# Kernel tuning notes

Measured on AMD Instinct MI355X. Metric: run time of the kernel, lower is better.

The kernel has to match this reference:

```python
import jax, jax.numpy as jnp
import numpy as np

TAU = 1.0
EPS = 1e-5


def _gcn_sparse(x, src, dst, ew, W, b, n):
    # PyG GCNConv: add self-loops (weight 1), sym-normalize, aggregate src->dst
    deg = jax.ops.segment_sum(ew, dst, num_segments=n) + 1.0
    dinv = jnp.where(deg > 0, jax.lax.rsqrt(deg), 0.0)
    h = x @ W
    coef = dinv[src] * ew * dinv[dst]              # [E]
    out = jax.ops.segment_sum(h[src] * coef[:, None], dst, num_segments=n)
    out = out + h * (dinv * dinv)[:, None]         # self-loop term
    return out + b


def _gcn_dense(x, A, W, b):
    # x: [B,N,d], A: [B,N,N] with A[b,i,j] = weight of edge j->i
    n = A.shape[-1]
    Ah = A + jnp.eye(n, dtype=A.dtype)
    deg = Ah.sum(-1)
    dinv = jnp.where(deg > 0, jax.lax.rsqrt(deg), 0.0)
    An = dinv[:, :, None] * Ah * dinv[:, None, :]
    return jnp.einsum('bij,bjd->bid', An, x @ W) + b


def _bn_silu(x, g, be, axes):
    # BatchNorm over node axis (training-mode batch stats, biased var) + SiLU
    m = x.mean(axes, keepdims=True)
    v = x.var(axes, keepdims=True)
    return jax.nn.silu(g * (x - m) * jax.lax.rsqrt(v + EPS) + be)


def setup_inputs() -> dict:
    key = jax.random.key(0)
    ks = jax.random.split(key, 12)
    B, NPG, EPER = 32, 1024, 16384
    CIN, C, K1, K2, OUT = 64, 128, 128, 32, 10
    N, E = B * NPG, B * EPER
    ei = jax.random.randint(ks[0], (2, E), 0, NPG, dtype=jnp.int32)
    off = jnp.repeat(jnp.arange(B, dtype=jnp.int32) * NPG, EPER)
    edge_index = ei + off[None, :]
    x = jax.random.normal(ks[1], (N, CIN), jnp.float32)
    batch = jnp.repeat(jnp.arange(B, dtype=jnp.int32), NPG)
    batch_ptr = jnp.arange(B + 1, dtype=jnp.int32) * NPG
    p = lambda k, s: jax.random.normal(k, s, jnp.float32) * 0.05
    return dict(
        x=x, edge_index=edge_index, batch=batch, batch_ptr=batch_ptr,
        w1a=p(ks[2], (CIN, C)), b1a=jnp.zeros((C,)), g1a=jnp.ones((C,)), be1a=jnp.zeros((C,)),
        w1b=p(ks[3], (C, C)), b1b=jnp.zeros((C,)), g1b=jnp.ones((C,)), be1b=jnp.zeros((C,)),
        wp1=p(ks[4], (C, K1)), bp1=jnp.zeros((K1,)),
        w2a=p(ks[5], (C, C)), b2a=jnp.zeros((C,)), g2a=jnp.ones((C,)), be2a=jnp.zeros((C,)),
        w2b=p(ks[6], (C, C)), b2b=jnp.zeros((C,)), g2b=jnp.ones((C,)), be2b=jnp.zeros((C,)),
        wp2=p(ks[7], (C, K2)), bp2=jnp.zeros((K2,)),
        wl=p(ks[8], (C, OUT)), bl=jnp.zeros((OUT,)))


def reference(x, edge_index, batch, batch_ptr,
              w1a, b1a, g1a, be1a, w1b, b1b, g1b, be1b, wp1, bp1,
              w2a, b2a, g2a, be2a, w2b, b2b, g2b, be2b, wp2, bp2,
              wl, bl):
    n = x.shape[0]
    B = batch_ptr.shape[0] - 1
    npg = n // B                                    # uniform nodes per graph
    src, dst = edge_index[0], edge_index[1]
    ew = jnp.ones((edge_index.shape[1],), x.dtype)  # edge_weight=None -> ones

    # ---- stack 1: sparse GCN residual blocks + stochastic pool ----
    h = _bn_silu(_gcn_sparse(x, src, dst, ew, w1a, b1a, n), g1a, be1a, 0)
    h = h + _bn_silu(_gcn_sparse(h, src, dst, ew, w1b, b1b, n), g1b, be1b, 0)
    s = jax.nn.softmax(_gcn_sparse(h, src, dst, ew, wp1, bp1, n) / TAU, -1)  # [n,K1]
    s3 = s.reshape(B, npg, -1)
    x2 = jnp.einsum('bnc,bnd->bcd', s3, h.reshape(B, npg, -1))   # s^T x  [B,K1,C]
    t = jax.ops.segment_sum(s[src] * ew[:, None], dst, num_segments=n)  # A s
    A2 = jnp.einsum('bnc,bnk->bck', s3, t.reshape(B, npg, -1))   # s^T A s [B,K1,K1]

    # ---- stack 2: dense GCN on pooled graph + stochastic pool ----
    h2 = _bn_silu(_gcn_dense(x2, A2, w2a, b2a), g2a, be2a, (0, 1))
    h2 = h2 + _bn_silu(_gcn_dense(h2, A2, w2b, b2b), g2b, be2b, (0, 1))
    s2 = jax.nn.softmax(_gcn_dense(h2, A2, wp2, bp2) / TAU, -1)  # [B,K1,K2]
    x3 = jnp.einsum('bnc,bnd->bcd', s2, h2)                      # [B,K2,C]

    # global mean pool over nodes per graph, linear, log_softmax
    g = x3.mean(axis=1)
    out = jax.nn.log_softmax(g @ wl + bl, axis=1)
    # aux losses are multiplied by 0 in the original forward -> exact zero
    return (out, jnp.zeros((), x.dtype))
```

## Files before the change

### kernel.cpp

```cpp
#include <hip/hip_runtime.h>
#include <cmath>

#define KSPLIT 8
#define ELL_ST 80

typedef __attribute__((ext_vector_type(8))) short short8;
typedef __attribute__((ext_vector_type(4))) float float4v;

static __device__ __forceinline__ unsigned short f2bf(float f){
  union { float f; unsigned u; } c; c.f = f;
  unsigned r = c.u + 0x7fff + ((c.u >> 16) & 1);
  return (unsigned short)(r >> 16);
}
static __device__ __forceinline__ float u2f(unsigned u){
  union { unsigned u; float f; } c; c.u = u; return c.f;
}
static __device__ __forceinline__ float silu(float y){ return y/(1.f+__expf(-y)); }

static __device__ __forceinline__ void coef_prologue(const float* __restrict__ stats,
                                                     const float* __restrict__ gamma,
                                                     const float* __restrict__ beta,
                                                     float invM, float* lds, int tbase){
  int t = threadIdx.x - tbase;
  if(t >= 0 && t < 128){
    float s = 0.f, q = 0.f;
    #pragma unroll
    for(int k=0;k<8;k++){ s += stats[k*128+t]; q += stats[1024 + k*128+t]; }
    float m = s*invM;
    float v = q*invM - m*m;
    float sc = gamma[t]*rsqrtf(v + 1e-5f);
    lds[t] = sc;
    lds[128+t] = beta[t] - m*sc;
  }
}

__global__ void k_fill_wt(const int* __restrict__ src, const int* __restrict__ dst,
                          int* __restrict__ cursor, int* __restrict__ esrc, int E,
                          const float* __restrict__ w1a, const float* __restrict__ w1b,
                          const float* __restrict__ wp1, const float* __restrict__ w2a,
                          const float* __restrict__ w2b,
                          unsigned short* __restrict__ t1a, unsigned short* __restrict__ t1b,
                          unsigned short* __restrict__ tp1, unsigned short* __restrict__ t2a,
                          unsigned short* __restrict__ t2b,
                          const float* __restrict__ xin, unsigned short* __restrict__ xb,
                          int NX, int CIN){
  int i = blockIdx.x*256 + threadIdx.x;
  if(i < E){
    int d = dst[i];
    int p = atomicAdd(&cursor[d], 1);
    if(p < ELL_ST) esrc[(size_t)d*ELL_ST + p] = src[i];
  } else {
    int j = i - E;
    int n1 = CIN*128, n2 = 128*128;
    if(j >= 0 && j < n1){
      int k = j >> 7, c = j & 127;
      t1a[(size_t)c*CIN + k] = f2bf(w1a[j]);
    } else if(j >= n1 && j < n1+n2){
      int jj = j - n1; int k = jj >> 7, c = jj & 127;
      t1b[(size_t)c*128 + k] = f2bf(w1b[jj]);
    } else if(j >= n1+n2 && j < n1+2*n2){
      int jj = j - n1 - n2; int k = jj >> 7, c = jj & 127;
      tp1[(size_t)c*128 + k] = f2bf(wp1[jj]);
    } else if(j >= n1+2*n2 && j < n1+3*n2){
      int jj = j - n1 - 2*n2; int k = jj >> 7, c = jj & 127;
      t2a[(size_t)c*128 + k] = f2bf(w2a[jj]);
    } else if(j >= n1+3*n2 && j < n1+4*n2){
      int jj = j - n1 - 3*n2; int k = jj >> 7, c = jj & 127;
      t2b[(size_t)c*128 + k] = f2bf(w2b[jj]);
    } else if(j >= n1+4*n2 && j < n1+4*n2+NX){
      int jj = j - n1 - 4*n2;
      xb[jj] = f2bf(xin[jj]);
    }
  }
}

template<bool ABF16>
__global__ void k_gemm_mfma(const void* __restrict__ A, const void* __restrict__ A2,
                            const unsigned short* __restrict__ Bt,
                            unsigned short* __restrict__ Cb,
                            unsigned short* __restrict__ Hout, int M, int K,
                            const int* __restrict__ rowdeg,
                            const float* __restrict__ rowscale,
                            const float* __restrict__ stA, const float* __restrict__ gA,
                            const float* __restrict__ beA,
                            const float* __restrict__ stB, const float* __restrict__ gB,
                            const float* __restrict__ beB, float invM){
  __shared__ unsigned short Abf[64][40];
  __shared__ unsigned short Bbf[128][40];
  __shared__ float lcA[256], lcB[256];
  int tid = threadIdx.x;
  if(stA) coef_prologue(stA, gA, beA, invM, lcA, 0);
  if(stB) coef_prologue(stB, gB, beB, invM, lcB, 128);
  if(stA || stB) __syncthreads();
  int wv = tid >> 6, lane = tid & 63;
  int quad = lane >> 4, l16 = lane & 15;
  int row0 = blockIdx.x*64;
  int sr = tid >> 2, sk = (tid & 3)*8;
  int srb = tid >> 1, skb = (tid & 1)*16;
  float4v acc[8] = {};
  for(int kt=0; kt<K; kt+=32){
    uint4 pk;
    if(ABF16){
      const unsigned short* ap = (const unsigned short*)A + (size_t)(row0+sr)*K + kt + sk;
      uint4 u = *(const uint4*)ap;
      if(stA){
        float va[8];
        va[0]=u2f(u.x<<16); va[1]=u2f(u.x&0xffff0000u);
        va[2]=u2f(u.y<<16); va[3]=u2f(u.y&0xffff0000u);
        va[4]=u2f(u.z<<16); va[5]=u2f(u.z&0xffff0000u);
        va[6]=u2f(u.w<<16); va[7]=u2f(u.w&0xffff0000u);
        if(stB){
          const unsigned short* bp = (const unsigned short*)A2 + (size_t)(row0+sr)*K + kt + sk;
          uint4 v = *(const uint4*)bp;
          float vb[8];
          vb[0]=u2f(v.x<<16); vb[1]=u2f(v.x&0xffff0000u);
          vb[2]=u2f(v.y<<16); vb[3]=u2f(v.y&0xffff0000u);
          vb[4]=u2f(v.z<<16); vb[5]=u2f(v.z&0xffff0000u);
          vb[6]=u2f(v.w<<16); vb[7]=u2f(v.w&0xffff0000u);
          #pragma unroll
          for(int i=0;i<8;i++){
            int c = kt+sk+i;
            va[i] = silu(lcA[c]*va[i] + lcA[128+c]) + silu(lcB[c]*vb[i] + lcB[128+c]);
          }
        } else {
          #pragma unroll
          for(int i=0;i<8;i++){
            int c = kt+sk+i;
            va[i] = silu(lcA[c]*va[i] + lcA[128+c]);
          }
        }
        pk.x = (unsigned)f2bf(va[0]) | ((unsigned)f2bf(va[1])<<16);
        pk.y = (unsigned)f2bf(va[2]) | ((unsigned)f2bf(va[3])<<16);
        pk.z = (unsigned)f2bf(va[4]) | ((unsigned)f2bf(va[5])<<16);
        pk.w = (unsigned)f2bf(va[6]) | ((unsigned)f2bf(va[7])<<16);
      } else {
        pk = u;
      }
    } else {
      const float* ap = (const float*)A + (size_t)(row0+sr)*K + kt + sk;
      float va[8];
      *(float4*)&va[0] = *(const float4*)ap;
      *(float4*)&va[4] = *(const float4*)(ap+4);
      if(stA){
        #pragma unroll
        for(int i=0;i<8;i++){
          int c = kt+sk+i;
          va[i] = silu(lcA[c]*va[i] + lcA[128+c]);
        }
      }
      pk.x = (unsigned)f2bf(va[0]) | ((unsigned)f2bf(va[1])<<16);
      pk.y = (unsigned)f2bf(va[2]) | ((unsigned)f2bf(va[3])<<16);
      pk.z = (unsigned)f2bf(va[4]) | ((unsigned)f2bf(va[5])<<16);
      pk.w = (unsigned)f2bf(va[6]) | ((unsigned)f2bf(va[7])<<16);
    }
    *(uint4*)&Abf[sr][sk] = pk;
    if(Hout)
      *(uint4*)&Hout[(size_t)(row0+sr)*128 + kt + sk] = pk;
    *(uint4*)&Bbf[srb][skb]   = *(const uint4*)&Bt[(size_t)srb*K + kt + skb];
    *(uint4*)&Bbf[srb][skb+8] = *(const uint4*)&Bt[(size_t)srb*K + kt + skb + 8];
    __syncthreads();
    short8 af = *(const short8*)&Abf[wv*16 + l16][quad*8];
    #pragma unroll
    for(int t=0;t<8;t++){
      short8 bf = *(const short8*)&Bbf[t*16 + l16][quad*8];
      acc[t] = __builtin_amdgcn_mfma_f32_16x16x32_bf16(af, bf, acc[t], 0, 0, 0);
    }
    __syncthreads();
  }
  float scr[4];
  #pragma unroll
  for(int r=0;r<4;r++){
    int grow = row0 + wv*16 + quad*4 + r;
    scr[r] = rowdeg ? rsqrtf((float)rowdeg[grow] + 1.0f) : (rowscale ? rowscale[grow] : 1.f);
  }
  #pragma unroll
  for(int t=0;t<8;t++){
    #pragma unroll
    for(int r=0;r<4;r++){
      int grow = row0 + wv*16 + quad*4 + r;
      Cb[(size_t)grow*128 + t*16 + l16] = f2bf(acc[t][r]*scr[r]);
    }
  }
}

template<bool DO_SOFTMAX, bool GCN, bool STATS, bool BF16IN, bool BF16OUT>
__global__ void k_gather(const int* __restrict__ degc, const int* __restrict__ esrc,
                         const void* __restrict__ hWs,
                         const float* __restrict__ bias, float* __restrict__ out,
                         float* __restrict__ stats){
  __shared__ float lsum[4][128];
  __shared__ float lsq[4][128];
  const unsigned short* h16 = (const unsigned short*)hWs;
  const float* h32 = (const float*)hWs;
  int wave = threadIdx.x >> 6;
  int lane = threadIdx.x & 63;
  int bid = blockIdx.x;
  int d = ((bid & 7) << 12) | ((bid >> 3) << 2) | wave;
  int grp = lane >> 5;
  int c4 = (lane & 31)*4;
  int dgr = degc[d];
  int cnt = dgr > ELL_ST ? ELL_ST : dgr;
  cnt = __builtin_amdgcn_readfirstlane(cnt);
  const int* row = esrc + (size_t)d*ELL_ST;

  auto loadrow = [&](int s)->float4{
    if(BF16IN){
      uint2 u = *(const uint2*)&h16[(size_t)s*128 + c4];
      float4 v;
      v.x = u2f(u.x << 16); v.y = u2f(u.x & 0xffff0000u);
      v.z = u2f(u.y << 16); v.w = u2f(u.y & 0xffff0000u);
      return v;
    } else {
      return *(const float4*)&h32[(size_t)s*128 + c4];
    }
  };

  float4 a0 = {0.f,0.f,0.f,0.f}, a1 = {0.f,0.f,0.f,0.f};
  float4 a2 = {0.f,0.f,0.f,0.f}, a3 = {0.f,0.f,0.f,0.f};
  if(GCN && grp == 0)
    a0 = loadrow(d);
  for(int base=0; base<cnt; base+=32){
    int m = cnt - base; if(m > 32) m = 32;
    int idx = (lane < m) ? row[base + lane] : 0;
    int full = m & ~7;
    int j0 = 0;
    for(; j0 < full; j0 += 8){
      int s0 = __shfl(idx, j0+grp);
      int s1 = __shfl(idx, j0+grp+2);
      int s2 = __shfl(idx, j0+grp+4);
      int s3 = __shfl(idx, j0+grp+6);
      float4 v0 = loadrow(s0);
      float4 v1 = loadrow(s1);
      float4 v2 = loadrow(s2);
      float4 v3 = loadrow(s3);
      a0.x+=v0.x; a0.y+=v0.y; a0.z+=v0.z; a0.w+=v0.w;
      a1.x+=v1.x; a1.y+=v1.y; a1.z+=v1.z; a1.w+=v1.w;
      a2.x+=v2.x; a2.y+=v2.y; a2.z+=v2.z; a2.w+=v2.w;
      a3.x+=v3.x; a3.y+=v3.y; a3.z+=v3.z; a3.w+=v3.w;
    }
    if(j0 < m){
      int jj0 = j0+grp, jj1 = j0+grp+2, jj2 = j0+grp+4, jj3 = j0+grp+6;
      int s0 = __shfl(idx, jj0 < m ? jj0 : 0);
      int s1 = __shfl(idx, jj1 < m ? jj1 : 0);
      int s2 = __shfl(idx, jj2 < m ? jj2 : 0);
      int s3 = __shfl(idx, jj3 < m ? jj3 : 0);
      if(jj0 < m){ float4 v = loadrow(s0);
        a0.x+=v.x; a0.y+=v.y; a0.z+=v.z; a0.w+=v.w; }
      if(jj1 < m){ float4 v = loadrow(s1);
        a1.x+=v.x; a1.y+=v.y; a1.z+=v.z; a1.w+=v.w; }
      if(jj2 < m){ float4 v = loadrow(s2);
        a2.x+=v.x; a2.y+=v.y; a2.z+=v.z; a2.w+=v.w; }
      if(jj3 < m){ float4 v = loadrow(s3);
        a3.x+=v.x; a3.y+=v.y; a3.z+=v.z; a3.w+=v.w; }
    }
  }
  float4 acc;
  acc.x = (a0.x+a1.x)+(a2.x+a3.x);
  acc.y = (a0.y+a1.y)+(a2.y+a3.y);
  acc.z = (a0.z+a1.z)+(a2.z+a3.z);
  acc.w = (a0.w+a1.w)+(a2.w+a3.w);
  acc.x += __shfl_xor(acc.x, 32);
  acc.y += __shfl_xor(acc.y, 32);
  acc.z += __shfl_xor(acc.z, 32);
  acc.w += __shfl_xor(acc.w, 32);
  float4 val = acc;
  if(GCN){
    float dv = rsqrtf((float)dgr + 1.0f);
    float4 bi = *(const float4*)&bias[c4];
    val.x = dv*acc.x + bi.x; val.y = dv*acc.y + bi.y;
    val.z = dv*acc.z + bi.z; val.w = dv*acc.w + bi.w;
  }
  if(DO_SOFTMAX){
    float mx = fmaxf(fmaxf(val.x,val.y), fmaxf(val.z,val.w));
    #pragma unroll
    for(int o=1;o<32;o<<=1) mx = fmaxf(mx, __shfl_xor(mx,o));
    float4 e; e.x=__expf(val.x-mx); e.y=__expf(val.y-mx);
    e.z=__expf(val.z-mx); e.w=__expf(val.w-mx);
    float s = e.x+e.y+e.z+e.w;
    #pragma unroll
    for(int o=1;o<32;o<<=1) s += __shfl_xor(s,o);
    float inv = 1.f/s;
    val.x=e.x*inv; val.y=e.y*inv; val.z=e.z*inv; val.w=e.w*inv;
  }
  if(grp == 0){
    if(BF16OUT){
      unsigned short* o16 = (unsigned short*)out;
      uint2 w;
      w.x = (unsigned)f2bf(val.x) | ((unsigned)f2bf(val.y)<<16);
      w.y = (unsigned)f2bf(val.z) | ((unsigned)f2bf(val.w)<<16);
      *(uint2*)&o16[(size_t)d*128 + c4] = w;
    } else {
      *(float4*)&out[(size_t)d*128 + c4] = val;
    }
  }
  if(STATS){
    if(grp == 0){
      *(float4*)&lsum[wave][c4] = val;
      float4 q; q.x=val.x*val.x; q.y=val.y*val.y; q.z=val.z*val.z; q.w=val.w*val.w;
      *(float4*)&lsq[wave][c4] = q;
    }
    __syncthreads();
    int t = threadIdx.x;
    if(t < 128){
      float s = (lsum[0][t]+lsum[1][t]) + (lsum[2][t]+lsum[3][t]);
      atomicAdd(&stats[(bid & 7)*128 + t], s);
    } else {
      int c = t - 128;
      float q = (lsq[0][c]+lsq[1][c]) + (lsq[2][c]+lsq[3][c]);
      atomicAdd(&stats[1024 + (bid & 7)*128 + c], q);
    }
  }
}

__global__ __launch_bounds__(256, 2)
void k_pool2(const unsigned short* __restrict__ P, const unsigned short* __restrict__ QH,
             const unsigned short* __restrict__ QT,
             float* __restrict__ part1, float* __restrict__ part2, int npg, int nb){
  __shared__ unsigned short sT[128][40];
  __shared__ unsigned short qT[128][40];
  int tid = threadIdx.x;
  bool zq = (blockIdx.z == 0);
  const unsigned short* Q = zq ? QH : QT;
  int ks = blockIdx.x, b = blockIdx.y;
  int klen = npg / KSPLIT;
  size_t base = ((size_t)b*npg + (size_t)ks*klen)*128;
  int wv = tid >> 6, lane = tid & 63;
  int quad = lane >> 4, l16 = lane & 15;
  int wr = (wv >> 1)*64, wc = (wv & 1)*64;
  int arr = tid >> 7;
  int t7 = tid & 127;
  int sg = (t7 >> 4)*16;
  int sr2 = (t7 & 15)*2;
  float4v acc[4][4] = {};

  for(int c0 = 0; c0 < klen; c0 += 32){
    size_t i0 = base + (size_t)(c0+sr2)*128 + sg;
    const unsigned short* Sp = arr ? Q : P;
    unsigned short (*dstT)[40] = arr ? qT : sT;
    uint4 ua = *(const uint4*)&Sp[i0];
    uint4 ub = *(const uint4*)&Sp[i0+8];
    uint4 uc = *(const uint4*)&Sp[i0+128];
    uint4 ud = *(const uint4*)&Sp[i0+136];
    unsigned short lo[16], hi[16];
    *(uint4*)&lo[0]=ua; *(uint4*)&lo[8]=ub;
    *(uint4*)&hi[0]=uc; *(uint4*)&hi[8]=ud;
    #pragma unroll
    for(int j=0;j<16;j++)
      *(unsigned*)&dstT[sg+j][sr2] = (unsigned)lo[j] | ((unsigned)hi[j]<<16);
    __syncthreads();
    #pragma unroll
    for(int i=0;i<4;i++){
      short8 af = *(const short8*)&sT[wr + i*16 + l16][quad*8];
      #pragma unroll
      for(int j=0;j<4;j++){
        short8 bf = *(const short8*)&qT[wc + j*16 + l16][quad*8];
        acc[i][j] = __builtin_amdgcn_mfma_f32_16x16x32_bf16(af, bf, acc[i][j], 0, 0, 0);
      }
    }
    __syncthreads();
  }

  float* outp = (zq ? part1 : part2) + ((size_t)(ks*nb + b)*128)*128;
  #pragma unroll
  for(int i=0;i<4;i++)
    #pragma unroll
    for(int r=0;r<4;r++){
      int m = wr + i*16 + quad*4 + r;
      #pragma unroll
      for(int j=0;j<4;j++)
        outp[(size_t)m*128 + wc + j*16 + l16] = acc[i][j][r];
    }
}

__global__ void k_pool_reduce2(const float* __restrict__ p1, const float* __restrict__ p2,
                               float* __restrict__ x2, unsigned short* __restrict__ A2b,
                               float* __restrict__ dinv2, int total){
  int i = blockIdx.x*256 + threadIdx.x;
  int half = total >> 2;
  if(i < half){
    float4 s = *(const float4*)&p1[(size_t)i*4];
    #pragma unroll
    for(int ks=1; ks<KSPLIT; ks++){
      float4 v = *(const float4*)&p1[(size_t)ks*total + (size_t)i*4];
      s.x+=v.x; s.y+=v.y; s.z+=v.z; s.w+=v.w;
    }
    *(float4*)&x2[(size_t)i*4] = s;
  } else {
    int ia = i - half;
    float4 s = *(const float4*)&p2[(size_t)ia*4];
    #pragma unroll
    for(int ks=1; ks<KSPLIT; ks++){
      float4 v = *(const float4*)&p2[(size_t)ks*total + (size_t)ia*4];
      s.x+=v.x; s.y+=v.y; s.z+=v.z; s.w+=v.w;
    }
    uint2 w;
    w.x = (unsigned)f2bf(s.x) | ((unsigned)f2bf(s.y)<<16);
    w.y = (unsigned)f2bf(s.z) | ((unsigned)f2bf(s.w)<<16);
    *(uint2*)&A2b[(size_t)ia*4] = w;
    float rs = s.x+s.y+s.z+s.w;
    #pragma unroll
    for(int o=16;o>0;o>>=1) rs += __shfl_xor(rs, o);
    if((threadIdx.x & 31) == 0) dinv2[ia>>5] = rsqrtf(rs + 1.0f);
  }
}

__global__ void k_bgemm_mfma(const unsigned short* __restrict__ A2b,
                             const unsigned short* __restrict__ Xb,
                             const float* __restrict__ dinv2, const float* __restrict__ bias,
                             float* __restrict__ outp, float* __restrict__ stats){
  __shared__ unsigned short Al[128][40];
  __shared__ unsigned short Xt[128][40];
  __shared__ float ssum[128], ssq[128];
  int tid = threadIdx.x;
  int b = blockIdx.x;
  if(tid < 128){ ssum[tid] = 0.f; ssq[tid] = 0.f; }
  int wv = tid >> 6, lane = tid & 63;
  int quad = lane >> 4, l16 = lane & 15;
  int wr = (wv >> 1)*64, wc = (wv & 1)*64;
  int arr = tid >> 7;
  int t7 = tid & 127;
  int sg = (t7 >> 4)*16, sr2 = (t7 & 15)*2;
  float4v acc[4][4] = {};

  for(int n0 = 0; n0 < 128; n0 += 32){
    if(arr == 0){
      const unsigned short* ap = &A2b[((size_t)b*128 + t7)*128 + n0];
      *(uint4*)&Al[t7][0]  = *(const uint4*)&ap[0];
      *(uint4*)&Al[t7][8]  = *(const uint4*)&ap[8];
      *(uint4*)&Al[t7][16] = *(const uint4*)&ap[16];
      *(uint4*)&Al[t7][24] = *(const uint4*)&ap[24];
    } else {
      size_t i0 = ((size_t)(b*128 + n0 + sr2))*128 + sg;
      uint4 ua = *(const uint4*)&Xb[i0];
      uint4 ub = *(const uint4*)&Xb[i0+8];
      uint4 uc = *(const uint4*)&Xb[i0+128];
      uint4 ud = *(const uint4*)&Xb[i0+136];
      unsigned short lo[16], hi[16];
      *(uint4*)&lo[0]=ua; *(uint4*)&lo[8]=ub;
      *(uint4*)&hi[0]=uc; *(uint4*)&hi[8]=ud;
      #pragma unroll
      for(int j=0;j<16;j++)
        *(unsigned*)&Xt[sg+j][sr2] = (unsigned)lo[j] | ((unsigned)hi[j]<<16);
    }
    __syncthreads();
    #pragma unroll
    for(int i=0;i<4;i++){
      short8 af = *(const short8*)&Al[wr + i*16 + l16][quad*8];
      #pragma unroll
      for(int j=0;j<4;j++){
        short8 bf = *(const short8*)&Xt[wc + j*16 + l16][quad*8];
        acc[i][j] = __builtin_amdgcn_mfma_f32_16x16x32_bf16(af, bf, acc[i][j], 0, 0, 0);
      }
    }
    __syncthreads();
  }

  float sv[4] = {}, sq[4] = {};
  #pragma unroll
  for(int i=0;i<4;i++){
    #pragma unroll
    for(int r=0;r<4;r++){
      int m = wr + i*16 + quad*4 + r;
      float dv = dinv2[b*128 + m];
      #pragma unroll
      for(int j=0;j<4;j++){
        int c = wc + j*16 + l16;
        float xr = u2f((unsigned)Xb[((size_t)(b*128 + m))*128 + c] << 16);
        float v = dv*(acc[i][j][r] + xr) + bias[c];
        outp[((size_t)(b*128 + m))*128 + c] = v;
        sv[j] += v; sq[j] += v*v;
      }
    }
  }
  #pragma unroll
  for(int j=0;j<4;j++){
    int c = wc + j*16 + l16;
    atomicAdd(&ssum[c], sv[j]);
    atomicAdd(&ssq[c], sq[j]);
  }
  __syncthreads();
  if(tid < 128){
    int slot = b & 7;
    atomicAdd(&stats[slot*128 + tid], ssum[tid]);
    atomicAdd(&stats[1024 + slot*128 + tid], ssq[tid]);
  }
}

__global__ void k_final(const float* __restrict__ dTa, const float* __restrict__ dTb,
                        const float* __restrict__ stA, const float* __restrict__ gA,
                        const float* __restrict__ beA,
                        const float* __restrict__ stB, const float* __restrict__ gB,
                        const float* __restrict__ beB, float invMc,
                        const float* __restrict__ wl, const float* __restrict__ bl,
                        float* __restrict__ out, int K1n, int Cc, float inv_k2,
                        int OUTc, int zero_idx){
  __shared__ float lcA[256], lcB[256];
  __shared__ float red[256];
  __shared__ float gsh[128];
  __shared__ float logits[32];
  __shared__ float mred, lred;
  coef_prologue(stA, gA, beA, invMc, lcA, 0);
  coef_prologue(stB, gB, beB, invMc, lcB, 128);
  __syncthreads();
  int b = blockIdx.x;
  int tid = threadIdx.x;
  int c = tid & 127, rh = tid >> 7;
  const float* pa = dTa + (size_t)b*K1n*Cc;
  const float* pb = dTb + (size_t)b*K1n*Cc;
  float sa = lcA[c], ha = lcA[128+c], sb = lcB[c], hb = lcB[128+c];
  float acc = 0.f;
  for(int r = rh; r < K1n; r += 2){
    float ya = sa*pa[(size_t)r*Cc + c] + ha;
    float yb = sb*pb[(size_t)r*Cc + c] + hb;
    acc += silu(ya) + silu(yb);
  }
  red[tid] = acc;
  __syncthreads();
  if(tid < 128) gsh[tid] = (red[tid] + red[tid+128]) * inv_k2;
  __syncthreads();
  if(tid < OUTc){
    float l = bl[tid];
    for(int d=0; d<Cc; d++) l += gsh[d]*wl[d*OUTc + tid];
    logits[tid] = l;
  }
  __syncthreads();
  if(tid==0){
    float m = -1e30f;
    for(int o=0;o<OUTc;o++) m = fmaxf(m, logits[o]);
    float s = 0.f;
    for(int o=0;o<OUTc;o++) s += __expf(logits[o]-m);
    mred = m; lred = logf(s);
  }
  __syncthreads();
  if(tid < OUTc) out[b*OUTc + tid] = logits[tid] - mred - lred;
  if(b==0 && tid==0 && zero_idx >= 0) out[zero_idx] = 0.f;
}

extern "C" void kernel_launch(void* const* d_in, const int* in_sizes, int n_in,
                              void* d_out, int out_size, void* d_ws, size_t ws_size,
                              hipStream_t stream){
  const float* x    = (const float*)d_in[0];
  const int*   ei   = (const int*)d_in[1];
  const float* w1a  = (const float*)d_in[4];
  const float* b1a  = (const float*)d_in[5];
  const float* g1a  = (const float*)d_in[6];
  const float* be1a = (const float*)d_in[7];
  const float* w1b  = (const float*)d_in[8];
  const float* b1b  = (const float*)d_in[9];
  const float* g1b  = (const float*)d_in[10];
  const float* be1b = (const float*)d_in[11];
  const float* wp1  = (const float*)d_in[12];
  const float* bp1  = (const float*)d_in[13];
  const float* w2a  = (const float*)d_in[14];
  const float* b2a  = (const float*)d_in[15];
  const float* g2a  = (const float*)d_in[16];
  const float* be2a = (const float*)d_in[17];
  const float* w2b  = (const float*)d_in[18];
  const float* b2b  = (const float*)d_in[19];
  const float* g2b  = (const float*)d_in[20];
  const float* be2b = (const float*)d_in[21];
  const float* wl   = (const float*)d_in[24];
  const float* bl   = (const float*)d_in[25];
  float* out = (float*)d_out;

  const int C_   = in_sizes[5];
  const int CIN_ = in_sizes[4]/C_;
  const int N    = in_sizes[0]/CIN_;
  const int E    = in_sizes[1]/2;
  const int B_   = in_sizes[3]-1;
  const int NPG_ = N/B_;
  const int K1_  = in_sizes[13];
  const int K2_  = in_sizes[23];
  const int OUTc = in_sizes[25];
  const int M2   = B_*K1_;
  const int total = M2*C_;
  const int NX   = N*CIN_;

  const int* srcI = ei;
  const int* dstI = ei + E;

  float* ws = (float*)d_ws;
  size_t o = 0;
  unsigned short* bufW = (unsigned short*)(ws + o); o += (size_t)N*C_/2;
  unsigned short* bufA = (unsigned short*)(ws + o); o += (size_t)N*C_/2;
  unsigned short* bufB = (unsigned short*)(ws + o); o += (size_t)N*C_/2;
  unsigned short* bufS = (unsigned short*)(ws + o); o += (size_t)N*C_/2;
  unsigned short* bufT = (unsigned short*)(ws + o); o += (size_t)N*C_/2;
  unsigned short* bufH = (unsigned short*)(ws + o); o += (size_t)N*C_/2;
  unsigned short* xbf  = (unsigned short*)(ws + o); o += (size_t)NX/2 + 64;
  float* x2    = ws + o; o += (size_t)total;
  unsigned short* A2b = (unsigned short*)(ws + o); o += (size_t)total/2;
  float* dinv2 = ws + o; o += (size_t)M2;
  float* st1a  = ws + o; o += 2048;
  float* st1b  = ws + o; o += 2048;
  float* stDa  = ws + o; o += 2048;
  float* stDb  = ws + o; o += 2048;
  int* cursor  = (int*)(ws + o); o += (size_t)N;
  float* part  = ws + o; o += (size_t)KSPLIT*total;
  float* part2 = ws + o; o += (size_t)KSPLIT*total;
  unsigned short* Xb = (unsigned short*)part;
  float* dTa = part + (size_t)total;
  float* dTb = part + 2*(size_t)total;
  unsigned short* wt1a = (unsigned short*)(ws + o); o += (size_t)CIN_*C_/2 + 64;
  unsigned short* wt1b = (unsigned short*)(ws + o); o += (size_t)C_*C_/2 + 64;
  unsigned short* wtp1 = (unsigned short*)(ws + o); o += (size_t)C_*C_/2 + 64;
  unsigned short* wt2a = (unsigned short*)(ws + o); o += (size_t)C_*C_/2 + 64;
  unsigned short* wt2b = (unsigned short*)(ws + o); o += (size_t)C_*C_/2 + 64;
  int* esrc    = (int*)(ws + o); o += (size_t)N*ELL_ST;
  (void)ws_size; (void)n_in;

  dim3 blk256(256);
  auto g1 = [](int n){ return dim3((unsigned)((n+255)/256)); };
  const float invN = 1.0f/N, invM2 = 1.0f/M2;

  hipMemsetAsync(st1a, 0, (size_t)4*2048*sizeof(float) + (size_t)N*sizeof(int), stream);
  k_fill_wt<<<g1(E + CIN_*C_ + 4*C_*C_ + NX), blk256, 0, stream>>>(srcI, dstI, cursor, esrc, E,
      w1a, w1b, wp1, w2a, w2b, wt1a, wt1b, wtp1, wt2a, wt2b, x, xbf, NX, CIN_);

  dim3 gath((unsigned)(N/4));
  dim3 gmm((unsigned)(N/64));

  k_gemm_mfma<true><<<gmm, blk256, 0, stream>>>(xbf, nullptr, wt1a, bufW, nullptr, N, CIN_, cursor,
      nullptr, nullptr, nullptr, nullptr, nullptr, nullptr, nullptr, 0.f);
  k_gather<false,true,true,true,true><<<gath, blk256, 0, stream>>>(cursor, esrc, bufW, b1a, (float*)bufA, st1a);

  k_gemm_mfma<true><<<gmm, blk256, 0, stream>>>(bufA, nullptr, wt1b, bufW, nullptr, N, C_, cursor,
      nullptr, st1a, g1a, be1a, nullptr, nullptr, nullptr, invN);
  k_gather<false,true,true,true,true><<<gath, blk256, 0, stream>>>(cursor, esrc, bufW, b1b, (float*)bufB, st1b);

  k_gemm_mfma<true><<<gmm, blk256, 0, stream>>>(bufA, bufB, wtp1, bufW, bufH, N, C_, cursor,
      nullptr, st1a, g1a, be1a, st1b, g1b, be1b, invN);
  k_gather<true,true,false,true,true><<<gath, blk256, 0, stream>>>(cursor, esrc, bufW, bp1, (float*)bufS, nullptr);
  k_gather<false,false,false,true,true><<<gath, blk256, 0, stream>>>(cursor, esrc, bufS, nullptr, (float*)bufT, nullptr);

  k_pool2<<<dim3(KSPLIT, B_, 2), blk256, 0, stream>>>(bufS, bufH, bufT,
      part, part2, NPG_, B_);
  k_pool_reduce2<<<g1(total/2), blk256, 0, stream>>>(part, part2, x2, A2b, dinv2, total);

  k_gemm_mfma<false><<<dim3((unsigned)(M2/64)), blk256, 0, stream>>>(x2, nullptr, wt2a, Xb, nullptr,
      M2, C_, nullptr, dinv2, nullptr, nullptr, nullptr, nullptr, nullptr, nullptr, 0.f);
  k_bgemm_mfma<<<dim3((unsigned)B_), blk256, 0, stream>>>(A2b, Xb, dinv2, b2a, dTa, stDa);

  k_gemm_mfma<false><<<dim3((unsigned)(M2/64)), blk256, 0, stream>>>(dTa, nullptr, wt2b, Xb, nullptr,
      M2, C_, nullptr, dinv2, stDa, g2a, be2a, nullptr, nullptr, nullptr, invM2);
  k_bgemm_mfma<<<dim3((unsigned)B_), blk256, 0, stream>>>(A2b, Xb, dinv2, b2b, dTb, stDb);

  int zero_idx = (out_size > B_*OUTc) ? B_*OUTc : -1;
  k_final<<<dim3((unsigned)B_), blk256, 0, stream>>>(dTa, dTb,
      stDa, g2a, be2a, stDb, g2b, be2b, invM2, wl, bl, out, K1_, C_, 1.0f/K2_,
      OUTc, zero_idx);
}
```

Baseline: 361.2 us.

## Fuse pooled-graph feature GEMM and adjacency GEMM into one per-graph kernel

Replaces the separate x@W GEMM and adjacency batched GEMM for each dense GCN layer with one kernel, one block per graph. The block computes the transformed features, scales them by dinv, and keeps them transposed in shared memory for the adjacency multiply and the self-loop term, instead of writing them to global memory and reading them back. The BN+SiLU activation of the previous layer is applied while loading. BN statistic accumulation slots also go from 8 to 32 to spread atomic contention. The cost is only 32 blocks doing more serial work each, plus more shared memory per block.

```diff
diff --git a/kernel.cpp b/kernel.cpp
--- a/kernel.cpp
+++ b/kernel.cpp
@@ -3,6 +3,7 @@
 
 #define KSPLIT 8
 #define ELL_ST 80
+#define NSLOT 32
 
 typedef __attribute__((ext_vector_type(8))) short short8;
 typedef __attribute__((ext_vector_type(4))) float float4v;
@@ -25,7 +26,7 @@
   if(t >= 0 && t < 128){
     float s = 0.f, q = 0.f;
     #pragma unroll
-    for(int k=0;k<8;k++){ s += stats[k*128+t]; q += stats[1024 + k*128+t]; }
+    for(int k=0;k<NSLOT;k++){ s += stats[k*128+t]; q += stats[NSLOT*128 + k*128+t]; }
     float m = s*invM;
     float v = q*invM - m*m;
     float sc = gamma[t]*rsqrtf(v + 1e-5f);
@@ -301,13 +302,14 @@
     }
     __syncthreads();
     int t = threadIdx.x;
+    int slot = bid & (NSLOT-1);
     if(t < 128){
       float s = (lsum[0][t]+lsum[1][t]) + (lsum[2][t]+lsum[3][t]);
-      atomicAdd(&stats[(bid & 7)*128 + t], s);
+      atomicAdd(&stats[slot*128 + t], s);
     } else {
       int c = t - 128;
       float q = (lsq[0][c]+lsq[1][c]) + (lsq[2][c]+lsq[3][c]);
-      atomicAdd(&stats[1024 + (bid & 7)*128 + c], q);
+      atomicAdd(&stats[NSLOT*128 + slot*128 + c], q);
     }
   }
 }
@@ -404,52 +406,86 @@
   }
 }
 
-__global__ void k_bgemm_mfma(const unsigned short* __restrict__ A2b,
-                             const unsigned short* __restrict__ Xb,
-                             const float* __restrict__ dinv2, const float* __restrict__ bias,
-                             float* __restrict__ outp, float* __restrict__ stats){
-  __shared__ unsigned short Al[128][40];
-  __shared__ unsigned short Xt[128][40];
+template<bool ACT>
+__global__ void k_dense2(const float* __restrict__ Ain,
+                         const unsigned short* __restrict__ Wt,
+                         const unsigned short* __restrict__ A2b,
+                         const float* __restrict__ dinv2, const float* __restrict__ bias,
+                         const float* __restrict__ stA, const float* __restrict__ gA,
+                         const float* __restrict__ beA, float invM,
+                         float* __restrict__ outp, float* __restrict__ stats){
+  __shared__ unsigned short Abf[64][40];
+  __shared__ unsigned short Bbf[128][40];
+  __shared__ unsigned short Xt[128][136];
   __shared__ float ssum[128], ssq[128];
+  __shared__ float lc[256];
   int tid = threadIdx.x;
   int b = blockIdx.x;
+  if(ACT) coef_prologue(stA, gA, beA, invM, lc, 0);
   if(tid < 128){ ssum[tid] = 0.f; ssq[tid] = 0.f; }
+  __syncthreads();
   int wv = tid >> 6, lane = tid & 63;
   int quad = lane >> 4, l16 = lane & 15;
+  int sr = tid >> 2, sk = (tid & 3)*8;
+  int srb = tid >> 1, skb = (tid & 1)*16;
+
+  for(int half = 0; half < 2; half++){
+    float4v acc[8] = {};
+    for(int kt=0; kt<128; kt+=32){
+      const float* ap = &Ain[((size_t)b*128 + half*64 + sr)*128 + kt + sk];
+      float va[8];
+      *(float4*)&va[0] = *(const float4*)ap;
+      *(float4*)&va[4] = *(const float4*)(ap+4);
+      if(ACT){
+        #pragma unroll
+        for(int i=0;i<8;i++){
+          int c = kt+sk+i;
+          va[i] = silu(lc[c]*va[i] + lc[128+c]);
+        }
+      }
+      uint4 pk;
+      pk.x = (unsigned)f2bf(va[0]) | ((unsigned)f2bf(va[1])<<16);
+      pk.y = (unsigned)f2bf(va[2]) | ((unsigned)f2bf(va[3])<<16);
+      pk.z = (unsigned)f2bf(va[4]) | ((unsigned)f2bf(va[5])<<16);
+      pk.w = (unsigned)f2bf(va[6]) | ((unsigned)f2bf(va[7])<<16);
+      *(uint4*)&Abf[sr][sk] = pk;
+      *(uint4*)&Bbf[srb][skb]   = *(const uint4*)&Wt[(size_t)srb*128 + kt + skb];
+      *(uint4*)&Bbf[srb][skb+8] = *(const uint4*)&Wt[(size_t)srb*128 + kt + skb + 8];
+      __syncthreads();
+      short8 af = *(const short8*)&Abf[wv*16 + l16][quad*8];
+      #pragma unroll
+      for(int t=0;t<8;t++){
+        short8 bf = *(const short8*)&Bbf[t*16 + l16][quad*8];
+        acc[t] = __builtin_amdgcn_mfma_f32_16x16x32_bf16(af, bf, acc[t], 0, 0, 0);
+      }
+      __syncthreads();
+    }
+    #pragma unroll
+    for(int t=0;t<8;t++){
+      #pragma unroll
+      for(int r=0;r<4;r++){
+        int m = half*64 + wv*16 + quad*4 + r;
+        float dv = dinv2[b*128 + m];
+        Xt[t*16 + l16][m] = f2bf(acc[t][r]*dv);
+      }
+    }
+    __syncthreads();
+  }
+
   int wr = (wv >> 1)*64, wc = (wv & 1)*64;
-  int arr = tid >> 7;
-  int t7 = tid & 127;
-  int sg = (t7 >> 4)*16, sr2 = (t7 & 15)*2;
-  float4v acc[4][4] = {};
-
+  float4v acc2[4][4] = {};
   for(int n0 = 0; n0 < 128; n0 += 32){
-    if(arr == 0){
-      const unsigned short* ap = &A2b[((size_t)b*128 + t7)*128 + n0];
-      *(uint4*)&Al[t7][0]  = *(const uint4*)&ap[0];
-      *(uint4*)&Al[t7][8]  = *(const uint4*)&ap[8];
-      *(uint4*)&Al[t7][16] = *(const uint4*)&ap[16];
-      *(uint4*)&Al[t7][24] = *(const uint4*)&ap[24];
-    } else {
-      size_t i0 = ((size_t)(b*128 + n0 + sr2))*128 + sg;
-      uint4 ua = *(const uint4*)&Xb[i0];
-      uint4 ub = *(const uint4*)&Xb[i0+8];
-      uint4 uc = *(const uint4*)&Xb[i0+128];
-      uint4 ud = *(const uint4*)&Xb[i0+136];
-      unsigned short lo[16], hi[16];
-      *(uint4*)&lo[0]=ua; *(uint4*)&lo[8]=ub;
-      *(uint4*)&hi[0]=uc; *(uint4*)&hi[8]=ud;
-      #pragma unroll
-      for(int j=0;j<16;j++)
-        *(unsigned*)&Xt[sg+j][sr2] = (unsigned)lo[j] | ((unsigned)hi[j]<<16);
-    }
+    const unsigned short* ap = &A2b[((size_t)b*128 + (tid>>1))*128 + n0 + (tid&1)*16];
+    *(uint4*)&Bbf[tid>>1][(tid&1)*16]     = *(const uint4*)ap;
+    *(uint4*)&Bbf[tid>>1][(tid&1)*16 + 8] = *(const uint4*)(ap + 8);
     __syncthreads();
     #pragma unroll
     for(int i=0;i<4;i++){
-      short8 af = *(const short8*)&Al[wr + i*16 + l16][quad*8];
+      short8 af = *(const short8*)&Bbf[wr + i*16 + l16][quad*8];
       #pragma unroll
       for(int j=0;j<4;j++){
-        short8 bf = *(const short8*)&Xt[wc + j*16 + l16][quad*8];
-        acc[i][j] = __builtin_amdgcn_mfma_f32_16x16x32_bf16(af, bf, acc[i][j], 0, 0, 0);
+        short8 bf = *(const short8*)&Xt[wc + j*16 + l16][n0 + quad*8];
+        acc2[i][j] = __builtin_amdgcn_mfma_f32_16x16x32_bf16(af, bf, acc2[i][j], 0, 0, 0);
       }
     }
     __syncthreads();
@@ -465,8 +501,8 @@
       #pragma unroll
       for(int j=0;j<4;j++){
         int c = wc + j*16 + l16;
-        float xr = u2f((unsigned)Xb[((size_t)(b*128 + m))*128 + c] << 16);
-        float v = dv*(acc[i][j][r] + xr) + bias[c];
+        float xr = u2f((unsigned)Xt[c][m] << 16);
+        float v = dv*(acc2[i][j][r] + xr) + bias[c];
         outp[((size_t)(b*128 + m))*128 + c] = v;
         sv[j] += v; sq[j] += v*v;
       }
@@ -480,9 +516,9 @@
   }
   __syncthreads();
   if(tid < 128){
-    int slot = b & 7;
+    int slot = b & (NSLOT-1);
     atomicAdd(&stats[slot*128 + tid], ssum[tid]);
-    atomicAdd(&stats[1024 + slot*128 + tid], ssq[tid]);
+    atomicAdd(&stats[NSLOT*128 + slot*128 + tid], ssq[tid]);
   }
 }
 
@@ -591,14 +627,13 @@
   float* x2    = ws + o; o += (size_t)total;
   unsigned short* A2b = (unsigned short*)(ws + o); o += (size_t)total/2;
   float* dinv2 = ws + o; o += (size_t)M2;
-  float* st1a  = ws + o; o += 2048;
-  float* st1b  = ws + o; o += 2048;
-  float* stDa  = ws + o; o += 2048;
-  float* stDb  = ws + o; o += 2048;
+  float* st1a  = ws + o; o += 2*NSLOT*128;
+  float* st1b  = ws + o; o += 2*NSLOT*128;
+  float* stDa  = ws + o; o += 2*NSLOT*128;
+  float* stDb  = ws + o; o += 2*NSLOT*128;
   int* cursor  = (int*)(ws + o); o += (size_t)N;
   float* part  = ws + o; o += (size_t)KSPLIT*total;
   float* part2 = ws + o; o += (size_t)KSPLIT*total;
-  unsigned short* Xb = (unsigned short*)part;
   float* dTa = part + (size_t)total;
   float* dTb = part + 2*(size_t)total;
   unsigned short* wt1a = (unsigned short*)(ws + o); o += (size_t)CIN_*C_/2 + 64;
@@ -613,7 +648,7 @@
   auto g1 = [](int n){ return dim3((unsigned)((n+255)/256)); };
   const float invN = 1.0f/N, invM2 = 1.0f/M2;
 
-  hipMemsetAsync(st1a, 0, (size_t)4*2048*sizeof(float) + (size_t)N*sizeof(int), stream);
+  hipMemsetAsync(st1a, 0, (size_t)4*2*NSLOT*128*sizeof(float) + (size_t)N*sizeof(int), stream);
   k_fill_wt<<<g1(E + CIN_*C_ + 4*C_*C_ + NX), blk256, 0, stream>>>(srcI, dstI, cursor, esrc, E,
       w1a, w1b, wp1, w2a, w2b, wt1a, wt1b, wtp1, wt2a, wt2b, x, xbf, NX, CIN_);
 
@@ -637,13 +672,10 @@
       part, part2, NPG_, B_);
   k_pool_reduce2<<<g1(total/2), blk256, 0, stream>>>(part, part2, x2, A2b, dinv2, total);
 
-  k_gemm_mfma<false><<<dim3((unsigned)(M2/64)), blk256, 0, stream>>>(x2, nullptr, wt2a, Xb, nullptr,
-      M2, C_, nullptr, dinv2, nullptr, nullptr, nullptr, nullptr, nullptr, nullptr, 0.f);
-  k_bgemm_mfma<<<dim3((unsigned)B_), blk256, 0, stream>>>(A2b, Xb, dinv2, b2a, dTa, stDa);
-
-  k_gemm_mfma<false><<<dim3((unsigned)(M2/64)), blk256, 0, stream>>>(dTa, nullptr, wt2b, Xb, nullptr,
-      M2, C_, nullptr, dinv2, stDa, g2a, be2a, nullptr, nullptr, nullptr, invM2);
-  k_bgemm_mfma<<<dim3((unsigned)B_), blk256, 0, stream>>>(A2b, Xb, dinv2, b2b, dTb, stDb);
+  k_dense2<false><<<dim3((unsigned)B_), blk256, 0, stream>>>(x2, wt2a, A2b, dinv2, b2a,
+      nullptr, nullptr, nullptr, 0.f, dTa, stDa);
+  k_dense2<true><<<dim3((unsigned)B_), blk256, 0, stream>>>(dTa, wt2b, A2b, dinv2, b2b,
+      stDa, g2a, be2a, invM2, dTb, stDb);
 
   int zero_idx = (out_size > B_*OUTc) ? B_*OUTc : -1;
   k_final<<<dim3((unsigned)B_), blk256, 0, stream>>>(dTa, dTb,
```

Measured after the change: 323.9 us. 10.3% less time.
